# Kernel optimization log

Hardware: AMD Instinct MI355X
Metric: run time of the kernel (lower is better)

Reference implementation:

```python
import jax, jax.numpy as jnp
import numpy as np

B = 1_000_000
FEAT = 64
EMBEDDING_SIZE = 128


def setup_inputs() -> dict:
    key = jax.random.key(0)
    k0, k1, k2 = jax.random.split(key, 3)
    x = jax.random.normal(k0, (B, FEAT), dtype=jnp.float32)
    W1 = jax.random.normal(k1, (FEAT, FEAT), dtype=jnp.float32) * (1.0 / np.sqrt(FEAT))
    b1 = jnp.zeros((FEAT,), dtype=jnp.float32)
    W2 = jax.random.normal(k2, (FEAT, EMBEDDING_SIZE), dtype=jnp.float32) * (1.0 / np.sqrt(FEAT))
    b2 = jnp.zeros((EMBEDDING_SIZE,), dtype=jnp.float32)
    return {"x": x, "W1": W1, "b1": b1, "W2": W2, "b2": b2}


def reference(x, W1, b1, W2, b2):
    # head: Linear(64,64) -> ReLU -> Linear(64, EMBEDDING_SIZE)
    h = jax.nn.relu(x @ W1 + b1)
    e = h @ W2 + b2
    # per-sample L2 normalize with zero-norm guard (Normalize module)
    norm = jnp.linalg.norm(e, axis=-1, keepdims=True)  # [B,1]
    out = jnp.where(norm == 0, jnp.zeros_like(e), e / jnp.where(norm == 0, 1.0, norm))
    return out
```

## Files before the change

### kernel.cpp

```cpp
#include <hip/hip_runtime.h>
#include <stdint.h>


typedef __attribute__((ext_vector_type(8))) short short8;
typedef __attribute__((ext_vector_type(4))) float f32x4;

#define TILES_PER_BLOCK 5

__device__ __forceinline__ ushort f2bf(float f) {
    union { float f; uint32_t u; } v; v.f = f;
    uint32_t u = v.u;
    u += 0x7fffu + ((u >> 16) & 1u);
    return (ushort)(u >> 16);
}
__device__ __forceinline__ uint32_t pack2(float a, float b) {
    return (uint32_t)f2bf(a) | ((uint32_t)f2bf(b) << 16);
}

__global__ __launch_bounds__(256)
void fused_head_kernel(const float* __restrict__ x,
                       const float* __restrict__ W1,
                       const float* __restrict__ b1,
                       const float* __restrict__ W2,
                       const float* __restrict__ b2,
                       float* __restrict__ out,
                       int ntiles)
{
    __shared__ ushort w1t[64][72];
    __shared__ ushort w2t[128][72];
    __shared__ ushort htile[4][16][72];
    __shared__ __align__(16) float b1s[64];
    __shared__ __align__(16) float b2s[128];

    const int tid  = threadIdx.x;
    const int wave = tid >> 6;
    const int lane = tid & 63;
    const int l16  = lane & 15;
    const int lq   = lane >> 4;

    const int t0   = blockIdx.x * TILES_PER_BLOCK;
    if (t0 >= ntiles) return;
    const int tcnt = (ntiles - t0 < TILES_PER_BLOCK) ? (ntiles - t0) : TILES_PER_BLOCK;

    const float* px = x + ((size_t)(t0 * 64 + wave * 16 + l16)) * 64 + lq * 8;

    f32x4 u[4];
    u[0] = *(const f32x4*)px;        u[1] = *(const f32x4*)(px + 4);
    u[2] = *(const f32x4*)(px + 32); u[3] = *(const f32x4*)(px + 36);

    for (int idx = tid; idx < 64 * 64; idx += 256) {
        int k = idx >> 6, n = idx & 63;
        w1t[n][k] = f2bf(W1[idx]);
    }
    for (int idx = tid; idx < 64 * 128; idx += 256) {
        int k = idx >> 7, n = idx & 127;
        w2t[n][k] = f2bf(W2[idx]);
    }
    if (tid < 64)  b1s[tid] = b1[tid];
    if (tid < 128) b2s[tid] = b2[tid];
    __syncthreads();

    for (int i = 0; i < tcnt; ++i) {
        const int t = t0 + i;

        short8 xf[2];
#pragma unroll
        for (int h = 0; h < 2; ++h) {
            short8 v;
            v[0] = (short)f2bf(u[2*h][0]);   v[1] = (short)f2bf(u[2*h][1]);
            v[2] = (short)f2bf(u[2*h][2]);   v[3] = (short)f2bf(u[2*h][3]);
            v[4] = (short)f2bf(u[2*h+1][0]); v[5] = (short)f2bf(u[2*h+1][1]);
            v[6] = (short)f2bf(u[2*h+1][2]); v[7] = (short)f2bf(u[2*h+1][3]);
            xf[h] = v;
        }

        if (i + 1 < tcnt) {
            const float* p = px + (size_t)(i + 1) * 4096;
            u[0] = *(const f32x4*)p;        u[1] = *(const f32x4*)(p + 4);
            u[2] = *(const f32x4*)(p + 32); u[3] = *(const f32x4*)(p + 36);
        }

        f32x4 acc1[4] = {};
#pragma unroll
        for (int h = 0; h < 2; ++h)
#pragma unroll
            for (int nt = 0; nt < 4; ++nt) {
                short8 wf = *(const short8*)&w1t[nt * 16 + l16][h * 32 + lq * 8];
                acc1[nt] = __builtin_amdgcn_mfma_f32_16x16x32_bf16(wf, xf[h], acc1[nt], 0, 0, 0);
            }

#pragma unroll
        for (int nt = 0; nt < 4; ++nt) {
            f32x4 bv = *(const f32x4*)&b1s[nt * 16 + lq * 4];
            float h0 = acc1[nt][0] + bv[0]; h0 = h0 > 0.f ? h0 : 0.f;
            float h1 = acc1[nt][1] + bv[1]; h1 = h1 > 0.f ? h1 : 0.f;
            float h2 = acc1[nt][2] + bv[2]; h2 = h2 > 0.f ? h2 : 0.f;
            float h3 = acc1[nt][3] + bv[3]; h3 = h3 > 0.f ? h3 : 0.f;
            uint32_t* dst = (uint32_t*)&htile[wave][l16][nt * 16 + lq * 4];
            dst[0] = pack2(h0, h1);
            dst[1] = pack2(h2, h3);
        }

        f32x4 acc2[8] = {};
#pragma unroll
        for (int h = 0; h < 2; ++h) {
            short8 hf = *(const short8*)&htile[wave][l16][h * 32 + lq * 8];
#pragma unroll
            for (int nt = 0; nt < 8; ++nt) {
                short8 wf = *(const short8*)&w2t[nt * 16 + l16][h * 32 + lq * 8];
                acc2[nt] = __builtin_amdgcn_mfma_f32_16x16x32_bf16(wf, hf, acc2[nt], 0, 0, 0);
            }
        }

        float ss = 0.f;
#pragma unroll
        for (int nt = 0; nt < 8; ++nt) {
            f32x4 bv = *(const f32x4*)&b2s[nt * 16 + lq * 4];
#pragma unroll
            for (int r = 0; r < 4; ++r) {
                float e = acc2[nt][r] + bv[r];
                acc2[nt][r] = e;
                ss += e * e;
            }
        }
        ss += __shfl_xor(ss, 16, 64);
        ss += __shfl_xor(ss, 32, 64);
        float sc = ss > 0.f ? rsqrtf(ss) : 0.f;

        float* po = out + ((size_t)(t * 64 + wave * 16 + l16)) * 128 + lq * 4;
#pragma unroll
        for (int nt = 0; nt < 8; ++nt) {
            f32x4 v;
            v[0] = acc2[nt][0] * sc; v[1] = acc2[nt][1] * sc;
            v[2] = acc2[nt][2] * sc; v[3] = acc2[nt][3] * sc;
            __builtin_nontemporal_store(v, (f32x4*)(po + nt * 16));
        }
    }
}

extern "C" void kernel_launch(void* const* d_in, const int* in_sizes, int n_in,
                              void* d_out, int out_size, void* d_ws, size_t ws_size,
                              hipStream_t stream) {
    const float* x  = (const float*)d_in[0];
    const float* W1 = (const float*)d_in[1];
    const float* b1 = (const float*)d_in[2];
    const float* W2 = (const float*)d_in[3];
    const float* b2 = (const float*)d_in[4];
    float* out = (float*)d_out;

    const int nrows  = in_sizes[0] / 64;
    const int ntiles = nrows / 64;
    const int grid   = (ntiles + TILES_PER_BLOCK - 1) / TILES_PER_BLOCK;

    hipLaunchKernelGGL(fused_head_kernel, dim3(grid), dim3(256), 0, stream,
                       x, W1, b1, W2, b2, out, ntiles);
}
```

Measured before the change: 717.0 us.

## Use fixed grid with balanced tile ranges and nontemporal input loads

```diff
diff --git a/kernel.cpp b/kernel.cpp
--- a/kernel.cpp
+++ b/kernel.cpp
@@ -1,17 +1,16 @@
 #include <hip/hip_runtime.h>
+#include <hip/hip_bf16.h>
 #include <stdint.h>
 
 
 typedef __attribute__((ext_vector_type(8))) short short8;
 typedef __attribute__((ext_vector_type(4))) float f32x4;
 
-#define TILES_PER_BLOCK 5
+#define GRID_BLOCKS 1024
 
 __device__ __forceinline__ ushort f2bf(float f) {
-    union { float f; uint32_t u; } v; v.f = f;
-    uint32_t u = v.u;
-    u += 0x7fffu + ((u >> 16) & 1u);
-    return (ushort)(u >> 16);
+    __hip_bfloat16 h = __float2bfloat16(f);
+    return *reinterpret_cast<ushort*>(&h);
 }
 __device__ __forceinline__ uint32_t pack2(float a, float b) {
     return (uint32_t)f2bf(a) | ((uint32_t)f2bf(b) << 16);
@@ -38,15 +37,18 @@
     const int l16  = lane & 15;
     const int lq   = lane >> 4;
 
-    const int t0   = blockIdx.x * TILES_PER_BLOCK;
-    if (t0 >= ntiles) return;
-    const int tcnt = (ntiles - t0 < TILES_PER_BLOCK) ? (ntiles - t0) : TILES_PER_BLOCK;
+    const int t0   = (int)(((long long)blockIdx.x * ntiles) / GRID_BLOCKS);
+    const int t1   = (int)(((long long)(blockIdx.x + 1) * ntiles) / GRID_BLOCKS);
+    const int tcnt = t1 - t0;
+    if (tcnt <= 0) return;
 
     const float* px = x + ((size_t)(t0 * 64 + wave * 16 + l16)) * 64 + lq * 8;
 
     f32x4 u[4];
-    u[0] = *(const f32x4*)px;        u[1] = *(const f32x4*)(px + 4);
-    u[2] = *(const f32x4*)(px + 32); u[3] = *(const f32x4*)(px + 36);
+    u[0] = __builtin_nontemporal_load((const f32x4*)px);
+    u[1] = __builtin_nontemporal_load((const f32x4*)(px + 4));
+    u[2] = __builtin_nontemporal_load((const f32x4*)(px + 32));
+    u[3] = __builtin_nontemporal_load((const f32x4*)(px + 36));
 
     for (int idx = tid; idx < 64 * 64; idx += 256) {
         int k = idx >> 6, n = idx & 63;
@@ -76,8 +78,10 @@
 
         if (i + 1 < tcnt) {
             const float* p = px + (size_t)(i + 1) * 4096;
-            u[0] = *(const f32x4*)p;        u[1] = *(const f32x4*)(p + 4);
-            u[2] = *(const f32x4*)(p + 32); u[3] = *(const f32x4*)(p + 36);
+            u[0] = __builtin_nontemporal_load((const f32x4*)p);
+            u[1] = __builtin_nontemporal_load((const f32x4*)(p + 4));
+            u[2] = __builtin_nontemporal_load((const f32x4*)(p + 32));
+            u[3] = __builtin_nontemporal_load((const f32x4*)(p + 36));
         }
 
         f32x4 acc1[4] = {};
@@ -150,8 +154,7 @@
 
     const int nrows  = in_sizes[0] / 64;
     const int ntiles = nrows / 64;
-    const int grid   = (ntiles + TILES_PER_BLOCK - 1) / TILES_PER_BLOCK;
 
-    hipLaunchKernelGGL(fused_head_kernel, dim3(grid), dim3(256), 0, stream,
+    hipLaunchKernelGGL(fused_head_kernel, dim3(GRID_BLOCKS), dim3(256), 0, stream,
                        x, W1, b1, W2, b2, out, ntiles);
 }
```

Result: no change. 715.5 us (-0.2%).
